# Kernel tuning notes

Hardware: AMD Instinct MI355X
Metric: run time of the kernel (lower is better)

Reference implementation:

```python
import jax, jax.numpy as jnp
import numpy as np

E = 96   # embed_dim; num_heads = 96 -> head_dim = 1, scale = 1.0
P = 4    # patch size (in_features 48 = 3 * 4 * 4)
NW = 4   # n_windows (hardcoded in apply_window_msa)


def setup_inputs() -> dict:
    key = jax.random.key(0)
    ks = jax.random.split(key, 5)
    x = jax.random.normal(ks[0], (16, 3, 256, 256), dtype=jnp.float32)
    lin_w = jax.random.normal(ks[1], (E, 48), dtype=jnp.float32) * (1.0 / np.sqrt(48).astype(np.float32))
    lin_b = jnp.zeros((E,), jnp.float32)
    in_proj_w = jax.random.normal(ks[2], (3 * E, E), dtype=jnp.float32) * (1.0 / np.sqrt(E).astype(np.float32))
    in_proj_b = jnp.zeros((3 * E,), jnp.float32)
    out_proj_w = jax.random.normal(ks[3], (E, E), dtype=jnp.float32) * (1.0 / np.sqrt(E).astype(np.float32))
    out_proj_b = jnp.zeros((E,), jnp.float32)
    return dict(x=x, lin_w=lin_w, lin_b=lin_b, in_proj_w=in_proj_w,
                in_proj_b=in_proj_b, out_proj_w=out_proj_w, out_proj_b=out_proj_b)


def reference(x, lin_w, lin_b, in_proj_w, in_proj_b, out_proj_w, out_proj_b):
    N, C, H, W = x.shape
    Hp, Wp = H // P, W // P
    # patch_merging: torch unfold(2,P,P).unfold(3,P,P) -> [N,C,Hp,Wp,P,P] -> reshape
    patches = x.reshape(N, C, Hp, P, Wp, P).transpose(0, 1, 2, 4, 3, 5)
    patches = patches.reshape(N, C * P * P, Hp, Wp)  # [N, 48, Hp, Wp]
    # apply_linear_on_axis(axis=1): acts as a 1x1 projection 48 -> E
    emb = jnp.einsum('nchw,ec->nehw', patches, lin_w) + lin_b[None, :, None, None]
    # apply_window_msa: raw reshape [N,E,Hp,Wp] -> [N, 4, L, E] (memory-order, faithful to source)
    wh, ww = Hp // 2, Wp // 2
    L = wh * ww
    xw = emb.reshape(N, NW, L, E).transpose(1, 0, 2, 3)  # [4, N, L, E]
    # torch MHA with batch_first=False: seq dim = N (samples), batch dim = L
    qkv = jnp.einsum('wnle,fe->wnlf', xw, in_proj_w) + in_proj_b  # [4, N, L, 3E]
    q, k, v = jnp.split(qkv, 3, axis=-1)  # each [4, N, L, E]; E heads of dim 1
    # head_dim = 1 -> scale = 1.0; scores over the N (sample) axis
    scores = jnp.einsum('wslh,wtlh->wlhst', q, k)        # [4, L, 96, N, N]
    attn = jax.nn.softmax(scores, axis=-1)
    out = jnp.einsum('wlhst,wtlh->wslh', attn, v)        # [4, N, L, E]
    out = jnp.einsum('wnle,fe->wnlf', out, out_proj_w) + out_proj_b
    hidden = out.transpose(1, 0, 2, 3).reshape(N, E, Hp, Wp)  # raw reshape, faithful
    return hidden
```

## Files before the change

### kernel.cpp

```cpp
#include <hip/hip_runtime.h>

#define EMB_STRIDE 393216

typedef __attribute__((ext_vector_type(8))) short short8;
typedef __attribute__((ext_vector_type(4))) float f32x4;
typedef __attribute__((ext_vector_type(2))) __fp16 f16x2;

#define MFMA16 __builtin_amdgcn_mfma_f32_16x16x32_bf16
#define SCHED_PIN() __builtin_amdgcn_sched_barrier(0)

static __device__ __forceinline__ short bf16h(float v) {
    unsigned u = __builtin_bit_cast(unsigned, v);
    unsigned r = (u + 0x7FFFu + ((u >> 16) & 1u)) >> 16;
    return (short)r;
}
static __device__ __forceinline__ float bf16f(short s) {
    unsigned u = ((unsigned)(unsigned short)s) << 16;
    return __builtin_bit_cast(float, u);
}
static __device__ __forceinline__ unsigned packsplit(float v) {
    const short h = bf16h(v);
    const float d = v - bf16f(h);
    const unsigned lo = __builtin_bit_cast(unsigned, d) >> 16;
    return ((unsigned)(unsigned short)h << 16) | lo;
}

__global__ __launch_bounds__(256) void k_prep(
    const float* __restrict__ lin_w, const float* __restrict__ in_w,
    const float* __restrict__ out_w,
    short* __restrict__ WH, short* __restrict__ WL2,
    short* __restrict__ WOH, short* __restrict__ WOL,
    short* __restrict__ WPH, short* __restrict__ WPL) {
    const int i0 = blockIdx.x * 256 + threadIdx.x;
    const int stride = gridDim.x * 256;
    for (int i = i0; i < 27648; i += stride) {
        int j = i & 7, g = (i >> 3) & 3, rest = i >> 5;
        int f = rest % 288, kc = rest / 288;
        float v = in_w[f * 96 + kc * 32 + g * 8 + j];
        short h = bf16h(v);
        WH[i] = h; WL2[i] = bf16h(v - bf16f(h));
    }
    for (int i = i0; i < 9216; i += stride) {
        int j = i & 7, g = (i >> 3) & 3, rest = i >> 5;
        int f = rest % 96, kc = rest / 96;
        float v = out_w[f * 96 + kc * 32 + g * 8 + j];
        short h = bf16h(v);
        WOH[i] = h; WOL[i] = bf16h(v - bf16f(h));
    }
    for (int i = i0; i < 6144; i += stride) {
        int j = i & 7, lane = (i >> 3) & 63, rest = i >> 9;
        int et = rest % 6, kc = rest / 6;
        int e = et * 16 + (lane & 15);
        int k = kc * 32 + (lane >> 4) * 8 + j;
        float v = (k < 48) ? lin_w[e * 48 + k] : 0.f;
        short h = bf16h(v);
        WPH[i] = h; WPL[i] = bf16h(v - bf16f(h));
    }
}

__global__ __launch_bounds__(256, 3) void k_patch(
    const float* __restrict__ x, const short* __restrict__ WPH,
    const short* __restrict__ WPL, const float* __restrict__ lin_b,
    unsigned* __restrict__ embp) {
    const int tid = threadIdx.x, wave = tid >> 6, lane = tid & 63;
    const int n = blockIdx.x >> 6;
    const int T = (blockIdx.x & 63) * 4 + wave;
    const int a = T >> 6, b = (T >> 2) & 15, cc = T & 3;
    const int col16 = lane & 15, grp = lane >> 4;
    const int d = col16 >> 2, g = col16 & 3;

    const int rowoff = (a * 4 + d) * 256 + b * 16 + cc * 4 + g;
    const int gA = (grp >> 1) * 65536 + (grp & 1) * 32768;
    const float* p0 = x + (size_t)n * 196608 + rowoff + gA;

    float v0[8], v1[8];
#pragma unroll
    for (int j = 0; j < 8; ++j) v0[j] = p0[j * 4096];
    if (grp < 2) {
#pragma unroll
        for (int j = 0; j < 8; ++j) v1[j] = p0[131072 - (grp >> 1) * 65536 + j * 4096];
    }
    SCHED_PIN();
    short8 Bh[2], Bl[2];
#pragma unroll
    for (int j = 0; j < 8; ++j) {
        const short h = bf16h(v0[j]);
        Bh[0][j] = h; Bl[0][j] = bf16h(v0[j] - bf16f(h));
        Bh[1][j] = 0; Bl[1][j] = 0;
    }
    if (grp < 2) {
#pragma unroll
        for (int j = 0; j < 8; ++j) {
            const short h = bf16h(v1[j]);
            Bh[1][j] = h; Bl[1][j] = bf16h(v1[j] - bf16f(h));
        }
    }

    f32x4 acc[6];
#pragma unroll
    for (int et = 0; et < 6; ++et) acc[et] = (f32x4){0.f, 0.f, 0.f, 0.f};
#pragma unroll
    for (int kc = 0; kc < 2; ++kc) {
        short8 AH[6], AL[6];
#pragma unroll
        for (int et = 0; et < 6; ++et)
            AH[et] = *(const short8*)(WPH + (kc * 6 + et) * 512 + lane * 8);
#pragma unroll
        for (int et = 0; et < 6; ++et)
            AL[et] = *(const short8*)(WPL + (kc * 6 + et) * 512 + lane * 8);
        SCHED_PIN();
#pragma unroll
        for (int et = 0; et < 6; ++et) acc[et] = MFMA16(AH[et], Bh[kc], acc[et], 0, 0, 0);
#pragma unroll
        for (int et = 0; et < 6; ++et) acc[et] = MFMA16(AH[et], Bl[kc], acc[et], 0, 0, 0);
#pragma unroll
        for (int et = 0; et < 6; ++et) acc[et] = MFMA16(AL[et], Bh[kc], acc[et], 0, 0, 0);
    }

    unsigned* ebase = embp + (size_t)n * EMB_STRIDE + T * 16 + col16;
#pragma unroll
    for (int et = 0; et < 6; ++et) {
        const float4 bv = *(const float4*)(lin_b + et * 16 + grp * 4);
        const float vr[4] = {acc[et][0] + bv.x, acc[et][1] + bv.y,
                             acc[et][2] + bv.z, acc[et][3] + bv.w};
#pragma unroll
        for (int r = 0; r < 4; ++r)
            ebase[(size_t)(et * 16 + grp * 4 + r) * 4096] = packsplit(vr[r]);
    }
}

__global__ __launch_bounds__(128, 2) void k_msa(
    const unsigned* __restrict__ embp,
    const short* __restrict__ WH, const short* __restrict__ WL2,
    const short* __restrict__ WOH, const short* __restrict__ WOL,
    const float* __restrict__ in_b, const float* __restrict__ out_b,
    float* __restrict__ out) {

    __shared__ unsigned KV[2][96 * 20];

    const int tid = threadIdx.x;
    const int half = tid >> 6, lane = tid & 63;
    const int wl0 = blockIdx.x * 2;
    const int n = lane & 15, g = lane >> 4;
    const int hoff = half * 1536;

    uint4 ub[12];
#pragma unroll
    for (int w = 0; w < 2; ++w) {
        const unsigned* xrow = embp + (size_t)n * EMB_STRIDE + (wl0 + w) * 96;
#pragma unroll
        for (int kc = 0; kc < 3; ++kc) {
            ub[(w * 3 + kc) * 2]     = *(const uint4*)(xrow + kc * 32 + g * 8);
            ub[(w * 3 + kc) * 2 + 1] = *(const uint4*)(xrow + kc * 32 + g * 8 + 4);
        }
    }
    SCHED_PIN();
    short8 Bh[2][3], Bl[2][3];
#pragma unroll
    for (int w = 0; w < 2; ++w)
#pragma unroll
        for (int kc = 0; kc < 3; ++kc) {
            const uint4 ua0 = ub[(w * 3 + kc) * 2], ua1 = ub[(w * 3 + kc) * 2 + 1];
            const unsigned ua[8] = {ua0.x, ua0.y, ua0.z, ua0.w, ua1.x, ua1.y, ua1.z, ua1.w};
#pragma unroll
            for (int j = 0; j < 8; ++j) {
                Bh[w][kc][j] = (short)(ua[j] >> 16);
                Bl[w][kc][j] = (short)(ua[j] & 0xffffu);
            }
        }

    f32x4 acc0[9], acc1[9];
#pragma unroll
    for (int a = 0; a < 9; ++a) {
        acc0[a] = (f32x4){0.f, 0.f, 0.f, 0.f};
        acc1[a] = (f32x4){0.f, 0.f, 0.f, 0.f};
    }
#pragma unroll
    for (int kc = 0; kc < 3; ++kc) {
        const short* whp = WH  + kc * 9216 + n * 32 + g * 8 + hoff;
        const short* wlp = WL2 + kc * 9216 + n * 32 + g * 8 + hoff;
        short8 AH[9], AL[9];
#pragma unroll
        for (int a = 0; a < 9; ++a)
            AH[a] = *(const short8*)(whp + ((a / 3) * 6 + (a % 3)) * 512);
#pragma unroll
        for (int a = 0; a < 9; ++a)
            AL[a] = *(const short8*)(wlp + ((a / 3) * 6 + (a % 3)) * 512);
        SCHED_PIN();
#pragma unroll
        for (int a = 0; a < 9; ++a) acc0[a] = MFMA16(AH[a], Bh[0][kc], acc0[a], 0, 0, 0);
#pragma unroll
        for (int a = 0; a < 9; ++a) acc1[a] = MFMA16(AH[a], Bh[1][kc], acc1[a], 0, 0, 0);
#pragma unroll
        for (int a = 0; a < 9; ++a) acc0[a] = MFMA16(AH[a], Bl[0][kc], acc0[a], 0, 0, 0);
#pragma unroll
        for (int a = 0; a < 9; ++a) acc1[a] = MFMA16(AH[a], Bl[1][kc], acc1[a], 0, 0, 0);
#pragma unroll
        for (int a = 0; a < 9; ++a) acc0[a] = MFMA16(AL[a], Bh[0][kc], acc0[a], 0, 0, 0);
#pragma unroll
        for (int a = 0; a < 9; ++a) acc1[a] = MFMA16(AL[a], Bh[1][kc], acc1[a], 0, 0, 0);
    }
#pragma unroll
    for (int a = 0; a < 9; ++a) {
        const float4 bv = *(const float4*)(in_b + ((a / 3) * 6 + (a % 3)) * 16 + half * 48 + g * 4);
        acc0[a][0] += bv.x; acc0[a][1] += bv.y; acc0[a][2] += bv.z; acc0[a][3] += bv.w;
        acc1[a][0] += bv.x; acc1[a][1] += bv.y; acc1[a][2] += bv.z; acc1[a][3] += bv.w;
    }

#pragma unroll
    for (int c = 0; c < 3; ++c)
#pragma unroll
        for (int r2 = 0; r2 < 4; ++r2) {
            const int h = half * 48 + c * 16 + g * 4 + r2;
            const f16x2 p0 = __builtin_amdgcn_cvt_pkrtz(acc0[3 + c][r2], acc0[6 + c][r2]);
            const f16x2 p1 = __builtin_amdgcn_cvt_pkrtz(acc1[3 + c][r2], acc1[6 + c][r2]);
            KV[0][h * 20 + n] = __builtin_bit_cast(unsigned, p0);
            KV[1][h * 20 + n] = __builtin_bit_cast(unsigned, p1);
        }

    unsigned ao0[12], ao1[12];
#define ATT_BODY(ACC, W, AOARR)                                                \
    {                                                                          \
        const float q2 = ACC[c][r2] * 1.44269504f;                             \
        const uint4* row = (const uint4*)(&KV[W][(half * 48 + c * 16 + g * 4 + r2) * 20]); \
        const uint4 ra = row[0], rb = row[1], rc = row[2], rd = row[3];        \
        const unsigned kv[16] = {ra.x, ra.y, ra.z, ra.w, rb.x, rb.y, rb.z, rb.w, \
                                 rc.x, rc.y, rc.z, rc.w, rd.x, rd.y, rd.z, rd.w}; \
        float sp[4] = {0.f, 0.f, 0.f, 0.f}, op[4] = {0.f, 0.f, 0.f, 0.f};      \
        _Pragma("unroll")                                                      \
        for (int tt = 0; tt < 16; ++tt) {                                      \
            const f16x2 kv2 = __builtin_bit_cast(f16x2, kv[tt]);               \
            const float e = __builtin_amdgcn_exp2f(q2 * (float)kv2[0]);        \
            sp[tt & 3] += e;                                                   \
            op[tt & 3] = fmaf(e, (float)kv2[1], op[tt & 3]);                   \
        }                                                                      \
        const float s = (sp[0] + sp[1]) + (sp[2] + sp[3]);                     \
        const float o = (op[0] + op[1]) + (op[2] + op[3]);                     \
        AOARR[c * 4 + r2] = packsplit(o * __builtin_amdgcn_rcpf(s));           \
    }
#pragma unroll
    for (int c = 0; c < 3; ++c)
#pragma unroll
        for (int r2 = 0; r2 < 4; ++r2) {
            ATT_BODY(acc0, 0, ao0)
            ATT_BODY(acc1, 1, ao1)
        }

#pragma unroll
    for (int c = 0; c < 3; ++c)
#pragma unroll
        for (int r2 = 0; r2 < 4; ++r2) {
            const int h = half * 48 + c * 16 + g * 4 + r2;
            KV[0][h * 20 + n] = ao0[c * 4 + r2];
            KV[1][h * 20 + n] = ao1[c * 4 + r2];
        }
    __syncthreads();

    f32x4 oc0[3], oc1[3];
#pragma unroll
    for (int c2 = 0; c2 < 3; ++c2) {
        oc0[c2] = (f32x4){0.f, 0.f, 0.f, 0.f};
        oc1[c2] = (f32x4){0.f, 0.f, 0.f, 0.f};
    }
#pragma unroll
    for (int kc = 0; kc < 3; ++kc) {
        const short* whp = WOH + kc * 3072 + n * 32 + g * 8 + hoff;
        const short* wlp = WOL + kc * 3072 + n * 32 + g * 8 + hoff;
        short8 OAH[3], OAL[3];
#pragma unroll
        for (int c2 = 0; c2 < 3; ++c2) OAH[c2] = *(const short8*)(whp + c2 * 512);
#pragma unroll
        for (int c2 = 0; c2 < 3; ++c2) OAL[c2] = *(const short8*)(wlp + c2 * 512);
        unsigned u0[8], u1[8];
#pragma unroll
        for (int j = 0; j < 8; ++j) {
            u0[j] = KV[0][(kc * 32 + g * 8 + j) * 20 + n];
            u1[j] = KV[1][(kc * 32 + g * 8 + j) * 20 + n];
        }
        SCHED_PIN();
        short8 bh0, bl0, bh1, bl1;
#pragma unroll
        for (int j = 0; j < 8; ++j) {
            bh0[j] = (short)(u0[j] >> 16); bl0[j] = (short)(u0[j] & 0xffffu);
            bh1[j] = (short)(u1[j] >> 16); bl1[j] = (short)(u1[j] & 0xffffu);
        }
#pragma unroll
        for (int c2 = 0; c2 < 3; ++c2) oc0[c2] = MFMA16(OAH[c2], bh0, oc0[c2], 0, 0, 0);
#pragma unroll
        for (int c2 = 0; c2 < 3; ++c2) oc1[c2] = MFMA16(OAH[c2], bh1, oc1[c2], 0, 0, 0);
#pragma unroll
        for (int c2 = 0; c2 < 3; ++c2) oc0[c2] = MFMA16(OAH[c2], bl0, oc0[c2], 0, 0, 0);
#pragma unroll
        for (int c2 = 0; c2 < 3; ++c2) oc1[c2] = MFMA16(OAH[c2], bl1, oc1[c2], 0, 0, 0);
#pragma unroll
        for (int c2 = 0; c2 < 3; ++c2) oc0[c2] = MFMA16(OAL[c2], bh0, oc0[c2], 0, 0, 0);
#pragma unroll
        for (int c2 = 0; c2 < 3; ++c2) oc1[c2] = MFMA16(OAL[c2], bh1, oc1[c2], 0, 0, 0);
    }

#pragma unroll
    for (int c2 = 0; c2 < 3; ++c2) {
        const int fb = half * 48 + c2 * 16 + g * 4;
        const float4 ob = *(const float4*)(out_b + fb);
        const float4 vs0 = make_float4(oc0[c2][0] + ob.x, oc0[c2][1] + ob.y,
                                       oc0[c2][2] + ob.z, oc0[c2][3] + ob.w);
        const float4 vs1 = make_float4(oc1[c2][0] + ob.x, oc1[c2][1] + ob.y,
                                       oc1[c2][2] + ob.z, oc1[c2][3] + ob.w);
        *(float4*)(out + (size_t)n * EMB_STRIDE + wl0 * 96 + fb) = vs0;
        *(float4*)(out + (size_t)n * EMB_STRIDE + (wl0 + 1) * 96 + fb) = vs1;
    }
}

extern "C" void kernel_launch(void* const* d_in, const int* in_sizes, int n_in,
                              void* d_out, int out_size, void* d_ws, size_t ws_size,
                              hipStream_t stream) {
    const float* x     = (const float*)d_in[0];
    const float* lin_w = (const float*)d_in[1];
    const float* lin_b = (const float*)d_in[2];
    const float* in_w  = (const float*)d_in[3];
    const float* in_b  = (const float*)d_in[4];
    const float* out_w = (const float*)d_in[5];
    const float* out_b = (const float*)d_in[6];
    float* outp = (float*)d_out;

    unsigned* embp = (unsigned*)d_ws;
    short* WH  = (short*)((char*)d_ws + 25165824);
    short* WL2 = WH + 32768;
    short* WOH = WH + 65536;
    short* WOL = WH + 81920;
    short* WPH = WH + 98304;
    short* WPL = WH + 106496;

    k_prep<<<64, 256, 0, stream>>>(lin_w, in_w, out_w, WH, WL2, WOH, WOL, WPH, WPL);
    k_patch<<<1024, 256, 0, stream>>>(x, WPH, WPL, lin_b, embp);
    k_msa<<<2048, 128, 0, stream>>>(embp, WH, WL2, WOH, WOL, in_b, out_b, outp);
}
```

Measured before the change: 66.12 us.

## Fold weight prep into patch kernel and split lin_w in-register

```diff
diff --git a/kernel.cpp b/kernel.cpp
--- a/kernel.cpp
+++ b/kernel.cpp
@@ -25,46 +25,36 @@
     return ((unsigned)(unsigned short)h << 16) | lo;
 }
 
-__global__ __launch_bounds__(256) void k_prep(
-    const float* __restrict__ lin_w, const float* __restrict__ in_w,
-    const float* __restrict__ out_w,
+__global__ __launch_bounds__(256, 3) void k_patch(
+    const float* __restrict__ x, const float* __restrict__ lin_w,
+    const float* __restrict__ lin_b, const float* __restrict__ in_w,
+    const float* __restrict__ out_w, unsigned* __restrict__ embp,
     short* __restrict__ WH, short* __restrict__ WL2,
-    short* __restrict__ WOH, short* __restrict__ WOL,
-    short* __restrict__ WPH, short* __restrict__ WPL) {
-    const int i0 = blockIdx.x * 256 + threadIdx.x;
-    const int stride = gridDim.x * 256;
-    for (int i = i0; i < 27648; i += stride) {
-        int j = i & 7, g = (i >> 3) & 3, rest = i >> 5;
-        int f = rest % 288, kc = rest / 288;
-        float v = in_w[f * 96 + kc * 32 + g * 8 + j];
-        short h = bf16h(v);
-        WH[i] = h; WL2[i] = bf16h(v - bf16f(h));
-    }
-    for (int i = i0; i < 9216; i += stride) {
-        int j = i & 7, g = (i >> 3) & 3, rest = i >> 5;
-        int f = rest % 96, kc = rest / 96;
-        float v = out_w[f * 96 + kc * 32 + g * 8 + j];
-        short h = bf16h(v);
-        WOH[i] = h; WOL[i] = bf16h(v - bf16f(h));
-    }
-    for (int i = i0; i < 6144; i += stride) {
-        int j = i & 7, lane = (i >> 3) & 63, rest = i >> 9;
-        int et = rest % 6, kc = rest / 6;
-        int e = et * 16 + (lane & 15);
-        int k = kc * 32 + (lane >> 4) * 8 + j;
-        float v = (k < 48) ? lin_w[e * 48 + k] : 0.f;
-        short h = bf16h(v);
-        WPH[i] = h; WPL[i] = bf16h(v - bf16f(h));
-    }
-}
-
-__global__ __launch_bounds__(256, 3) void k_patch(
-    const float* __restrict__ x, const short* __restrict__ WPH,
-    const short* __restrict__ WPL, const float* __restrict__ lin_b,
-    unsigned* __restrict__ embp) {
-    const int tid = threadIdx.x, wave = tid >> 6, lane = tid & 63;
-    const int n = blockIdx.x >> 6;
-    const int T = (blockIdx.x & 63) * 4 + wave;
+    short* __restrict__ WOH, short* __restrict__ WOL) {
+    const int bid = blockIdx.x;
+    const int tid = threadIdx.x;
+
+    if (bid >= 1024) {
+        for (int i = tid; i < 27648; i += 256) {
+            int j = i & 7, g = (i >> 3) & 3, rest = i >> 5;
+            int f = rest % 288, kc = rest / 288;
+            float v = in_w[f * 96 + kc * 32 + g * 8 + j];
+            short h = bf16h(v);
+            WH[i] = h; WL2[i] = bf16h(v - bf16f(h));
+        }
+        for (int i = tid; i < 9216; i += 256) {
+            int j = i & 7, g = (i >> 3) & 3, rest = i >> 5;
+            int f = rest % 96, kc = rest / 96;
+            float v = out_w[f * 96 + kc * 32 + g * 8 + j];
+            short h = bf16h(v);
+            WOH[i] = h; WOL[i] = bf16h(v - bf16f(h));
+        }
+        return;
+    }
+
+    const int wave = tid >> 6, lane = tid & 63;
+    const int n = bid >> 6;
+    const int T = (bid & 63) * 4 + wave;
     const int a = T >> 6, b = (T >> 2) & 15, cc = T & 3;
     const int col16 = lane & 15, grp = lane >> 4;
     const int d = col16 >> 2, g = col16 & 3;
@@ -101,14 +91,26 @@
     for (int et = 0; et < 6; ++et) acc[et] = (f32x4){0.f, 0.f, 0.f, 0.f};
 #pragma unroll
     for (int kc = 0; kc < 2; ++kc) {
+        float wv[6][8];
+        const bool valid = (kc == 0) | (grp < 2);
+#pragma unroll
+        for (int et = 0; et < 6; ++et) {
+            const float* wr = lin_w + (et * 16 + col16) * 48 + kc * 32 + grp * 8;
+            const float4 wa = valid ? *(const float4*)(wr)     : make_float4(0.f, 0.f, 0.f, 0.f);
+            const float4 wb = valid ? *(const float4*)(wr + 4) : make_float4(0.f, 0.f, 0.f, 0.f);
+            wv[et][0] = wa.x; wv[et][1] = wa.y; wv[et][2] = wa.z; wv[et][3] = wa.w;
+            wv[et][4] = wb.x; wv[et][5] = wb.y; wv[et][6] = wb.z; wv[et][7] = wb.w;
+        }
+        SCHED_PIN();
         short8 AH[6], AL[6];
 #pragma unroll
         for (int et = 0; et < 6; ++et)
-            AH[et] = *(const short8*)(WPH + (kc * 6 + et) * 512 + lane * 8);
-#pragma unroll
-        for (int et = 0; et < 6; ++et)
-            AL[et] = *(const short8*)(WPL + (kc * 6 + et) * 512 + lane * 8);
-        SCHED_PIN();
+#pragma unroll
+            for (int j = 0; j < 8; ++j) {
+                const short h = bf16h(wv[et][j]);
+                AH[et][j] = h;
+                AL[et][j] = bf16h(wv[et][j] - bf16f(h));
+            }
 #pragma unroll
         for (int et = 0; et < 6; ++et) acc[et] = MFMA16(AH[et], Bh[kc], acc[et], 0, 0, 0);
 #pragma unroll
@@ -328,10 +330,8 @@
     short* WL2 = WH + 32768;
     short* WOH = WH + 65536;
     short* WOL = WH + 81920;
-    short* WPH = WH + 98304;
-    short* WPL = WH + 106496;
-
-    k_prep<<<64, 256, 0, stream>>>(lin_w, in_w, out_w, WH, WL2, WOH, WOL, WPH, WPL);
-    k_patch<<<1024, 256, 0, stream>>>(x, WPH, WPL, lin_b, embp);
+
+    k_patch<<<1025, 256, 0, stream>>>(x, lin_w, lin_b, in_w, out_w,
+                                      embp, WH, WL2, WOH, WOL);
     k_msa<<<2048, 128, 0, stream>>>(embp, WH, WL2, WOH, WOL, in_b, out_b, outp);
 }
```

New measurement: 86.84 us. 31.3% more time.
